# Optimization experiments

Measured on AMD Instinct MI355X. Metric: run time of the kernel, lower is better.

The kernel has to match this reference:

```python
import jax, jax.numpy as jnp
import numpy as np

VOCAB, EMBED, HIDDEN, NCLASS = 50000, 256, 256, 5
B, T = 64, 512


def _lstm_cell(x, h, c, W, U, b):
    # Keras LSTMCell: gate order i, f, g(candidate), o
    z = x @ W + h @ U + b  # [B, 4H]
    i, f, g, o = jnp.split(z, 4, axis=-1)
    i = jax.nn.sigmoid(i)
    f = jax.nn.sigmoid(f)
    g = jnp.tanh(g)
    o = jax.nn.sigmoid(o)
    c_new = f * c + i * g
    h_new = o * jnp.tanh(c_new)
    return h_new, c_new


def _run_stacked(xs, W1, U1, b1, W2, U2, b2):
    # xs: [T, B, E] -> outputs of layer 2: [T, B, H]
    Bb = xs.shape[1]
    H = U1.shape[0]
    zero = jnp.zeros((Bb, H), dtype=xs.dtype)
    init = (zero, zero, zero, zero)

    def step(carry, x_t):
        h1, c1, h2, c2 = carry
        h1, c1 = _lstm_cell(x_t, h1, c1, W1, U1, b1)
        h2, c2 = _lstm_cell(h1, h2, c2, W2, U2, b2)
        return (h1, c1, h2, c2), h2

    _, ys = jax.lax.scan(step, init, xs)
    return ys


def setup_inputs() -> dict:
    key = jax.random.key(0)
    ks = jax.random.split(key, 16)
    s = 0.05

    def mk(k, shape):
        return (jax.random.normal(k, shape, dtype=jnp.float32) * s)

    inp = {
        "tokens": jax.random.randint(ks[0], (B, T), 0, VOCAB, dtype=jnp.int64),
        "embed_table": mk(ks[1], (VOCAB, EMBED)),
        # forward direction, layer 1 and 2
        "fw_W1": mk(ks[2], (EMBED, 4 * HIDDEN)),
        "fw_U1": mk(ks[3], (HIDDEN, 4 * HIDDEN)),
        "fw_b1": jnp.zeros((4 * HIDDEN,), jnp.float32),
        "fw_W2": mk(ks[4], (HIDDEN, 4 * HIDDEN)),
        "fw_U2": mk(ks[5], (HIDDEN, 4 * HIDDEN)),
        "fw_b2": jnp.zeros((4 * HIDDEN,), jnp.float32),
        # backward direction, layer 1 and 2
        "bw_W1": mk(ks[6], (EMBED, 4 * HIDDEN)),
        "bw_U1": mk(ks[7], (HIDDEN, 4 * HIDDEN)),
        "bw_b1": jnp.zeros((4 * HIDDEN,), jnp.float32),
        "bw_W2": mk(ks[8], (HIDDEN, 4 * HIDDEN)),
        "bw_U2": mk(ks[9], (HIDDEN, 4 * HIDDEN)),
        "bw_b2": jnp.zeros((4 * HIDDEN,), jnp.float32),
        # output dense (2H -> 5), softmax
        "dense_W": mk(ks[10], (2 * HIDDEN, NCLASS)),
        "dense_b": jnp.zeros((NCLASS,), jnp.float32),
    }
    return inp


def reference(tokens, embed_table,
              fw_W1, fw_U1, fw_b1, fw_W2, fw_U2, fw_b2,
              bw_W1, bw_U1, bw_b1, bw_W2, bw_U2, bw_b2,
              dense_W, dense_b):
    emb = embed_table[tokens]                    # [B, T, E]
    xs = jnp.swapaxes(emb, 0, 1)                 # [T, B, E]

    ys_fw = _run_stacked(xs, fw_W1, fw_U1, fw_b1, fw_W2, fw_U2, fw_b2)          # [T,B,H]
    ys_bw = _run_stacked(xs[::-1], bw_W1, bw_U1, bw_b1, bw_W2, bw_U2, bw_b2)[::-1]

    feat = jnp.concatenate([ys_fw, ys_bw], axis=-1)   # [T, B, 2H]
    feat = jnp.swapaxes(feat, 0, 1)                   # [B, T, 2H]
    logits = feat @ dense_W + dense_b                 # [B, T, 5]
    return jax.nn.softmax(logits, axis=-1)
```

## Files before the change

### kernel.cpp

```cpp
#include <hip/hip_runtime.h>

typedef __bf16 bf16;
typedef __bf16 bf16x8 __attribute__((ext_vector_type(8)));
typedef float f32x4 __attribute__((ext_vector_type(4)));
typedef unsigned long long u64;

#define T_LEN 512
#define BATCH 64
#define HID 256
#define LDA 520
#define ZLD 68

#define CTRL_BYTES 4096
#define LOG_OFF CTRL_BYTES
#define LOG_BYTES (T_LEN * BATCH * 5 * 4)
#define RING_OFF (LOG_OFF + LOG_BYTES)
#define HSLOT_U64 4096
#define RING_SLOTS 16
#define RING_U64 (RING_SLOTS * HSLOT_U64)
#define RING_BYTES (4 * RING_U64 * 8)

#define SMEM_A 66560
#define SMEM_Z 17408
#define SMEM_C 4096
#define SMEM_TAIL 576
#define SMEM_BYTES (SMEM_A + SMEM_Z + SMEM_C + SMEM_TAIL)

__device__ inline uint4 cvt8(const float4* s) {
    float4 a = s[0], b = s[1];
    union { uint4 u; bf16 h[8]; } r;
    r.h[0] = (bf16)a.x; r.h[1] = (bf16)a.y; r.h[2] = (bf16)a.z; r.h[3] = (bf16)a.w;
    r.h[4] = (bf16)b.x; r.h[5] = (bf16)b.y; r.h[6] = (bf16)b.z; r.h[7] = (bf16)b.w;
    return r.u;
}

__device__ __forceinline__ void poll16(const u64* src, int tid, unsigned ep, u64* dst) {
    unsigned todo = 0xffffu;
#pragma unroll
    for (int k = 0; k < 16; ++k)
        dst[k] = __hip_atomic_load(src + k * 256 + tid, __ATOMIC_RELAXED, __HIP_MEMORY_SCOPE_AGENT);
    for (;;) {
        unsigned rem = 0u;
#pragma unroll
        for (int k = 0; k < 16; ++k)
            if (((todo >> k) & 1u) && (((unsigned)dst[k]) & 1u) != ep) rem |= (1u << k);
        if (!rem) break;
        todo = rem;
#pragma unroll
        for (int k = 0; k < 16; ++k)
            if ((todo >> k) & 1u)
                dst[k] = __hip_atomic_load(src + k * 256 + tid, __ATOMIC_RELAXED, __HIP_MEMORY_SCOPE_AGENT);
    }
}

__global__ void __launch_bounds__(256, 1)
lstm_kernel(const int* __restrict__ tokens,
            const float* __restrict__ embed,
            const float* __restrict__ W1f, const float* __restrict__ U1f, const float* __restrict__ b1f,
            const float* __restrict__ W2f, const float* __restrict__ U2f, const float* __restrict__ b2f,
            const float* __restrict__ W1b, const float* __restrict__ U1b, const float* __restrict__ b1b,
            const float* __restrict__ W2b, const float* __restrict__ U2b, const float* __restrict__ b2b,
            const float* __restrict__ dW,
            char* __restrict__ ws)
{
    extern __shared__ char smem[];
    bf16*  Abuf  = (bf16*)smem;
    float* zLds  = (float*)(smem + SMEM_A);
    float* cLds  = (float*)(smem + SMEM_A + SMEM_Z);
    float* bLds  = (float*)(smem + SMEM_A + SMEM_Z + SMEM_C);
    float* dwLds = bLds + 64;

    const int tid = threadIdx.x;
    const int wg  = blockIdx.x;
    const int dir = wg & 1, layer = (wg >> 1) & 1, sub = wg >> 2;

    const float *Wp, *Up, *bp;
    if (dir == 0) { if (layer == 0) { Wp=W1f; Up=U1f; bp=b1f; } else { Wp=W2f; Up=U2f; bp=b2f; } }
    else          { if (layer == 0) { Wp=W1b; Up=U1b; bp=b1b; } else { Wp=W2b; Up=U2b; bp=b2b; } }

    {
        for (int it = 0; it < 32; ++it) {
            int idx = it * 256 + tid;
            int k = idx >> 4, q4 = idx & 15;
            int g = q4 >> 2, u0 = (q4 & 3) * 4;
            const float* src = (k < 256) ? (Wp + (size_t)k * 1024 + g * 256 + sub * 16 + u0)
                                         : (Up + (size_t)(k - 256) * 1024 + g * 256 + sub * 16 + u0);
            float4 v = *(const float4*)src;
            int c0 = g * 16 + u0;
            Abuf[(c0 + 0) * LDA + k] = (bf16)v.x;
            Abuf[(c0 + 1) * LDA + k] = (bf16)v.y;
            Abuf[(c0 + 2) * LDA + k] = (bf16)v.z;
            Abuf[(c0 + 3) * LDA + k] = (bf16)v.w;
        }
        if (tid < 64) {
            int g = tid >> 4, u = tid & 15;
            bLds[tid] = bp[g * 256 + sub * 16 + u];
        }
        if (tid < 80) {
            int u = tid / 5, c = tid % 5;
            dwLds[tid] = dW[(size_t)(dir * 256 + sub * 16 + u) * 5 + c];
        }
        for (int i = tid; i < 1024; i += 256) cLds[i] = 0.f;
    }
    __syncthreads();

    const int wave = tid >> 6, lane = tid & 63, quad = lane >> 4, ln = lane & 15;
    const int mrow0 = (wave >> 1) * 32, ncol0 = (wave & 1) * 32;
    bf16x8 bfrag[2][16];
#pragma unroll
    for (int nt = 0; nt < 2; ++nt)
#pragma unroll
        for (int kt = 0; kt < 16; ++kt)
            bfrag[nt][kt] = *(const bf16x8*)&Abuf[(ncol0 + nt * 16 + ln) * LDA + kt * 32 + quad * 8];
    __syncthreads();

    u64* ringL1  = (u64*)(ws + RING_OFF) + (size_t)(dir * 2 + 0) * RING_U64;
    u64* ringL2  = (u64*)(ws + RING_OFF) + (size_t)(dir * 2 + 1) * RING_U64;
    u64* ringOwn = (layer == 0) ? ringL1 : ringL2;
    float* logits  = (float*)(ws + LOG_OFF);
    unsigned* prog = (unsigned*)ws + dir * 32;

    const int bA = tid >> 2, qA = tid & 3;
    unsigned progCache = 0u;

    float4 pf[16];
    int tokB = 0;
    if (layer == 0) {
        const int tt0 = dir ? (T_LEN - 1) : 0;
        int tokA = tokens[bA * T_LEN + tt0];
        const float4* src = (const float4*)(embed + (size_t)tokA * HID + qA * 64);
#pragma unroll
        for (int j = 0; j < 16; ++j) pf[j] = src[j];
        const int tt1 = dir ? (T_LEN - 2) : 1;
        tokB = tokens[bA * T_LEN + tt1];
    }

    for (int s = 0; s < T_LEN; ++s) {
        if (layer == 0 && tid == 0 && s >= 13) {
            unsigned need = (unsigned)(s - 12);
            while (progCache < need)
                progCache = __hip_atomic_load(prog, __ATOMIC_RELAXED, __HIP_MEMORY_SCOPE_AGENT);
        }

        u64 hreg[16];
        if (s == 0) {
#pragma unroll
            for (int k = 0; k < 16; ++k) hreg[k] = 0ull;
        } else {
            poll16(ringOwn + (size_t)(s & 15) * HSLOT_U64, tid,
                   (unsigned)(((s - 1) >> 4) & 1), hreg);
        }

        if (layer == 0) {
            uint4* dstx = (uint4*)&Abuf[bA * LDA + qA * 64];
#pragma unroll
            for (int j = 0; j < 8; ++j) dstx[j] = cvt8(&pf[2 * j]);
        } else {
            u64 xreg[16];
            poll16(ringL1 + (size_t)((s + 1) & 15) * HSLOT_U64, tid,
                   (unsigned)((s >> 4) & 1), xreg);
#pragma unroll
            for (int k = 0; k < 16; ++k)
                *(u64*)&Abuf[bA * LDA + k * 16 + qA * 4] = xreg[k];
        }
#pragma unroll
        for (int k = 0; k < 16; ++k)
            *(u64*)&Abuf[bA * LDA + 256 + k * 16 + qA * 4] = hreg[k];
        __syncthreads();

        if (layer == 0) {
            const float4* src = (const float4*)(embed + (size_t)tokB * HID + qA * 64);
#pragma unroll
            for (int j = 0; j < 16; ++j) pf[j] = src[j];
            const int sn2 = (s + 2 < T_LEN) ? s + 2 : T_LEN - 1;
            const int tt2 = dir ? (T_LEN - 1 - sn2) : sn2;
            tokB = tokens[bA * T_LEN + tt2];
        }

        f32x4 acc[2][2];
#pragma unroll
        for (int mi = 0; mi < 2; ++mi)
#pragma unroll
            for (int ni = 0; ni < 2; ++ni) acc[mi][ni] = (f32x4)(0.0f);
#pragma unroll
        for (int kt = 0; kt < 16; ++kt) {
            bf16x8 a0 = *(const bf16x8*)&Abuf[(mrow0 + ln) * LDA + kt * 32 + quad * 8];
            bf16x8 a1 = *(const bf16x8*)&Abuf[(mrow0 + 16 + ln) * LDA + kt * 32 + quad * 8];
            acc[0][0] = __builtin_amdgcn_mfma_f32_16x16x32_bf16(a0, bfrag[0][kt], acc[0][0], 0, 0, 0);
            acc[0][1] = __builtin_amdgcn_mfma_f32_16x16x32_bf16(a0, bfrag[1][kt], acc[0][1], 0, 0, 0);
            acc[1][0] = __builtin_amdgcn_mfma_f32_16x16x32_bf16(a1, bfrag[0][kt], acc[1][0], 0, 0, 0);
            acc[1][1] = __builtin_amdgcn_mfma_f32_16x16x32_bf16(a1, bfrag[1][kt], acc[1][1], 0, 0, 0);
        }
#pragma unroll
        for (int mi = 0; mi < 2; ++mi)
#pragma unroll
            for (int ni = 0; ni < 2; ++ni) {
                int row = mrow0 + mi * 16 + quad * 4;
                int col = ncol0 + ni * 16 + ln;
#pragma unroll
                for (int r = 0; r < 4; ++r)
                    zLds[(row + r) * ZLD + col] = acc[mi][ni][r];
            }
        __syncthreads();

        u64* hdst = ringOwn + (size_t)((s + 1) & 15) * HSLOT_U64;
        float hv[4];
        {
            const int b = bA, u0 = qA * 4;
#pragma unroll
            for (int e = 0; e < 4; ++e) {
                int u = u0 + e;
                float zi = zLds[b * ZLD + u]      + bLds[u];
                float zf = zLds[b * ZLD + 16 + u] + bLds[16 + u];
                float zg = zLds[b * ZLD + 32 + u] + bLds[32 + u];
                float zo = zLds[b * ZLD + 48 + u] + bLds[48 + u];
                float ig = 1.f / (1.f + __expf(-zi));
                float fg = 1.f / (1.f + __expf(-zf));
                float gg = 1.f - 2.f / (__expf(2.f * zg) + 1.f);
                float og = 1.f / (1.f + __expf(-zo));
                float cn = fg * cLds[b * 16 + u] + ig * gg;
                cLds[b * 16 + u] = cn;
                hv[e] = og * (1.f - 2.f / (__expf(2.f * cn) + 1.f));
            }
            union { u64 w; bf16 h[4]; } pk;
#pragma unroll
            for (int e = 0; e < 4; ++e) pk.h[e] = (bf16)hv[e];
            pk.w = (pk.w & ~1ull) | (u64)((s >> 4) & 1);
            __hip_atomic_store(hdst + sub * 256 + tid, pk.w,
                               __ATOMIC_RELAXED, __HIP_MEMORY_SCOPE_AGENT);
        }
        float pr[5];
        if (layer == 1) {
#pragma unroll
            for (int c = 0; c < 5; ++c)
                pr[c] = hv[0] * dwLds[(qA * 4 + 0) * 5 + c] + hv[1] * dwLds[(qA * 4 + 1) * 5 + c]
                      + hv[2] * dwLds[(qA * 4 + 2) * 5 + c] + hv[3] * dwLds[(qA * 4 + 3) * 5 + c];
#pragma unroll
            for (int m = 1; m < 4; m <<= 1)
#pragma unroll
                for (int c = 0; c < 5; ++c) pr[c] += __shfl_xor(pr[c], m);
        }

        if (layer == 1 && tid == 0)
            __hip_atomic_store(prog, (unsigned)(s + 1),
                               __ATOMIC_RELAXED, __HIP_MEMORY_SCOPE_AGENT);

        if (layer == 1 && qA == 0) {
            const int tp = dir ? (T_LEN - 1 - s) : s;
            float* lp = &logits[((size_t)tp * BATCH + bA) * 5];
#pragma unroll
            for (int c = 0; c < 5; ++c) atomicAdd(lp + c, pr[c]);
        }
    }
}

__global__ void __launch_bounds__(256)
softmax_kernel(const char* __restrict__ ws, const float* __restrict__ dB, float* __restrict__ out)
{
    const int gid = blockIdx.x * 256 + threadIdx.x;
    const int b = gid & 63, t = gid >> 6;
    const float* lp = (const float*)(ws + LOG_OFF) + ((size_t)t * BATCH + b) * 5;
    float l[5];
#pragma unroll
    for (int c = 0; c < 5; ++c) l[c] = lp[c] + dB[c];
    float m = l[0];
#pragma unroll
    for (int c = 1; c < 5; ++c) m = fmaxf(m, l[c]);
    float e[5], ssum = 0.f;
#pragma unroll
    for (int c = 0; c < 5; ++c) { e[c] = __expf(l[c] - m); ssum += e[c]; }
    float inv = 1.f / ssum;
    float* o = out + ((size_t)b * T_LEN + t) * 5;
#pragma unroll
    for (int c = 0; c < 5; ++c) o[c] = e[c] * inv;
}

extern "C" void kernel_launch(void* const* d_in, const int* in_sizes, int n_in,
                              void* d_out, int out_size, void* d_ws, size_t ws_size,
                              hipStream_t stream)
{
    const int*   tokens = (const int*)d_in[0];
    const float* embed  = (const float*)d_in[1];
    const float* W1f = (const float*)d_in[2],  *U1f = (const float*)d_in[3],  *b1f = (const float*)d_in[4];
    const float* W2f = (const float*)d_in[5],  *U2f = (const float*)d_in[6],  *b2f = (const float*)d_in[7];
    const float* W1b = (const float*)d_in[8],  *U1b = (const float*)d_in[9],  *b1b = (const float*)d_in[10];
    const float* W2b = (const float*)d_in[11], *U2b = (const float*)d_in[12], *b2b = (const float*)d_in[13];
    const float* dW  = (const float*)d_in[14], *dB  = (const float*)d_in[15];

    hipFuncSetAttribute(reinterpret_cast<const void*>(lstm_kernel),
                        hipFuncAttributeMaxDynamicSharedMemorySize, SMEM_BYTES);
    hipMemsetAsync(d_ws, 0, RING_OFF, stream);
    hipMemsetAsync((char*)d_ws + RING_OFF, 0xFF, RING_BYTES, stream);
    lstm_kernel<<<dim3(64), dim3(256), SMEM_BYTES, stream>>>(
        tokens, embed, W1f, U1f, b1f, W2f, U2f, b2f,
        W1b, U1b, b1b, W2b, U2b, b2b, dW, (char*)d_ws);
    softmax_kernel<<<dim3(128), dim3(256), 0, stream>>>((const char*)d_ws, dB, (float*)d_out);
}
```

Before: 3.423 ms.

## Issue ring loads early, skip polling own slice, replace logit atomics with partial stores

The h and x ring loads are now issued before the progress wait, so their latency overlaps it. Polling becomes a wave-uniform retry with __all. Each block keeps its own h slice in a register instead of polling it back from global memory. The atomicAdd accumulation of dense logits is replaced by plain per-block partial stores that the softmax kernel sums, which removes atomic contention and the large memset. The cost is a 16x bigger logit buffer and whole-slot reloads whenever any lane is not ready.

```diff
diff --git a/kernel.cpp b/kernel.cpp
--- a/kernel.cpp
+++ b/kernel.cpp
@@ -13,7 +13,7 @@
 
 #define CTRL_BYTES 4096
 #define LOG_OFF CTRL_BYTES
-#define LOG_BYTES (T_LEN * BATCH * 5 * 4)
+#define LOG_BYTES (T_LEN * BATCH * 16 * 5 * 4)
 #define RING_OFF (LOG_OFF + LOG_BYTES)
 #define HSLOT_U64 4096
 #define RING_SLOTS 16
@@ -34,22 +34,21 @@
     return r.u;
 }
 
-__device__ __forceinline__ void poll16(const u64* src, int tid, unsigned ep, u64* dst) {
-    unsigned todo = 0xffffu;
+__device__ __forceinline__ void load16(const u64* src, int tid, u64* dst) {
 #pragma unroll
     for (int k = 0; k < 16; ++k)
         dst[k] = __hip_atomic_load(src + k * 256 + tid, __ATOMIC_RELAXED, __HIP_MEMORY_SCOPE_AGENT);
+}
+
+__device__ __forceinline__ void resolve16(const u64* src, int tid, unsigned ep,
+                                          unsigned mask, u64* dst) {
     for (;;) {
-        unsigned rem = 0u;
+        bool ok = true;
 #pragma unroll
         for (int k = 0; k < 16; ++k)
-            if (((todo >> k) & 1u) && (((unsigned)dst[k]) & 1u) != ep) rem |= (1u << k);
-        if (!rem) break;
-        todo = rem;
-#pragma unroll
-        for (int k = 0; k < 16; ++k)
-            if ((todo >> k) & 1u)
-                dst[k] = __hip_atomic_load(src + k * 256 + tid, __ATOMIC_RELAXED, __HIP_MEMORY_SCOPE_AGENT);
+            if ((mask >> k) & 1u) ok &= ((((unsigned)dst[k]) & 1u) == ep);
+        if (__all(ok)) break;
+        load16(src, tid, dst);
     }
 }
 
@@ -121,7 +120,9 @@
     unsigned* prog = (unsigned*)ws + dir * 32;
 
     const int bA = tid >> 2, qA = tid & 3;
+    const unsigned ownMask = 0xFFFFu ^ (1u << sub);
     unsigned progCache = 0u;
+    u64 pkPrevW = 0ull;
 
     float4 pf[16];
     int tokB = 0;
@@ -136,29 +137,32 @@
     }
 
     for (int s = 0; s < T_LEN; ++s) {
+        u64 hreg[16], xreg[16];
+        const u64* ownSrc = ringOwn + (size_t)(s & 15) * HSLOT_U64;
+        const u64* xSrc   = ringL1 + (size_t)((s + 1) & 15) * HSLOT_U64;
+        if (s > 0) load16(ownSrc, tid, hreg);
+        if (layer == 1) load16(xSrc, tid, xreg);
+
         if (layer == 0 && tid == 0 && s >= 13) {
             unsigned need = (unsigned)(s - 12);
             while (progCache < need)
                 progCache = __hip_atomic_load(prog, __ATOMIC_RELAXED, __HIP_MEMORY_SCOPE_AGENT);
         }
 
-        u64 hreg[16];
-        if (s == 0) {
+        if (s > 0) {
+            resolve16(ownSrc, tid, (unsigned)(((s - 1) >> 4) & 1), ownMask, hreg);
+        } else {
 #pragma unroll
             for (int k = 0; k < 16; ++k) hreg[k] = 0ull;
-        } else {
-            poll16(ringOwn + (size_t)(s & 15) * HSLOT_U64, tid,
-                   (unsigned)(((s - 1) >> 4) & 1), hreg);
-        }
+        }
+        hreg[sub] = pkPrevW;
 
         if (layer == 0) {
             uint4* dstx = (uint4*)&Abuf[bA * LDA + qA * 64];
 #pragma unroll
             for (int j = 0; j < 8; ++j) dstx[j] = cvt8(&pf[2 * j]);
         } else {
-            u64 xreg[16];
-            poll16(ringL1 + (size_t)((s + 1) & 15) * HSLOT_U64, tid,
-                   (unsigned)((s >> 4) & 1), xreg);
+            resolve16(xSrc, tid, (unsigned)((s >> 4) & 1), 0xFFFFu, xreg);
 #pragma unroll
             for (int k = 0; k < 16; ++k)
                 *(u64*)&Abuf[bA * LDA + k * 16 + qA * 4] = xreg[k];
@@ -226,6 +230,7 @@
 #pragma unroll
             for (int e = 0; e < 4; ++e) pk.h[e] = (bf16)hv[e];
             pk.w = (pk.w & ~1ull) | (u64)((s >> 4) & 1);
+            pkPrevW = pk.w;
             __hip_atomic_store(hdst + sub * 256 + tid, pk.w,
                                __ATOMIC_RELAXED, __HIP_MEMORY_SCOPE_AGENT);
         }
@@ -247,9 +252,9 @@
 
         if (layer == 1 && qA == 0) {
             const int tp = dir ? (T_LEN - 1 - s) : s;
-            float* lp = &logits[((size_t)tp * BATCH + bA) * 5];
-#pragma unroll
-            for (int c = 0; c < 5; ++c) atomicAdd(lp + c, pr[c]);
+            float* lp = &logits[(((size_t)tp * BATCH + bA) * 16 + sub) * 5];
+#pragma unroll
+            for (int c = 0; c < 5; ++c) lp[c] = pr[c];
         }
     }
 }
@@ -259,10 +264,14 @@
 {
     const int gid = blockIdx.x * 256 + threadIdx.x;
     const int b = gid & 63, t = gid >> 6;
-    const float* lp = (const float*)(ws + LOG_OFF) + ((size_t)t * BATCH + b) * 5;
+    const float* lp = (const float*)(ws + LOG_OFF) + ((size_t)t * BATCH + b) * 80;
     float l[5];
 #pragma unroll
-    for (int c = 0; c < 5; ++c) l[c] = lp[c] + dB[c];
+    for (int c = 0; c < 5; ++c) l[c] = dB[c];
+#pragma unroll
+    for (int sub = 0; sub < 16; ++sub)
+#pragma unroll
+        for (int c = 0; c < 5; ++c) l[c] += lp[sub * 5 + c];
     float m = l[0];
 #pragma unroll
     for (int c = 1; c < 5; ++c) m = fmaxf(m, l[c]);
@@ -289,7 +298,7 @@
 
     hipFuncSetAttribute(reinterpret_cast<const void*>(lstm_kernel),
                         hipFuncAttributeMaxDynamicSharedMemorySize, SMEM_BYTES);
-    hipMemsetAsync(d_ws, 0, RING_OFF, stream);
+    hipMemsetAsync(d_ws, 0, CTRL_BYTES, stream);
     hipMemsetAsync((char*)d_ws + RING_OFF, 0xFF, RING_BYTES, stream);
     lstm_kernel<<<dim3(64), dim3(256), SMEM_BYTES, stream>>>(
         tokens, embed, W1f, U1f, b1f, W2f, U2f, b2f,
```

Result: faster. 2.825 ms (-17.5%).
